# Kernel tuning notes

Hardware: AMD Instinct MI355X
Metric: run time of the kernel (lower is better)

## Reference

```python
import jax, jax.numpy as jnp
import numpy as np

DIM, HEADS, DFF = 768, 12, 3072
DK = DIM // HEADS
EPS = 1e-5

def _layernorm(x, w, b):
    mu = jnp.mean(x, axis=-1, keepdims=True)
    var = jnp.mean(jnp.square(x - mu), axis=-1, keepdims=True)
    return (x - mu) * jax.lax.rsqrt(var + EPS) * w + b

def setup_inputs() -> dict:
    key = jax.random.key(0)
    ks = jax.random.split(key, 5)
    B, N = 8, 1024
    std = 0.02
    return {
        "x": jax.random.normal(ks[0], (B, N, DIM), jnp.float32),
        "ln1_w": jnp.ones((DIM,), jnp.float32),
        "ln1_b": jnp.zeros((DIM,), jnp.float32),
        "qkv_w": jax.random.normal(ks[1], (3 * DIM, DIM), jnp.float32) * std,
        "qkv_b": jnp.zeros((3 * DIM,), jnp.float32),
        "proj_w": jax.random.normal(ks[2], (DIM, DIM), jnp.float32) * std,
        "proj_b": jnp.zeros((DIM,), jnp.float32),
        "ln2_w": jnp.ones((DIM,), jnp.float32),
        "ln2_b": jnp.zeros((DIM,), jnp.float32),
        "fc1_w": jax.random.normal(ks[3], (DFF, DIM), jnp.float32) * std,
        "fc1_b": jnp.zeros((DFF,), jnp.float32),
        "fc2_w": jax.random.normal(ks[4], (DIM, DFF), jnp.float32) * std,
        "fc2_b": jnp.zeros((DIM,), jnp.float32),
    }

def reference(x, ln1_w, ln1_b, qkv_w, qkv_b, proj_w, proj_b,
              ln2_w, ln2_b, fc1_w, fc1_b, fc2_w, fc2_b):
    B, N, C = x.shape
    # --- attention branch (pre-norm) ---
    h = _layernorm(x, ln1_w, ln1_b)
    qkv = h @ qkv_w.T + qkv_b                      # [B,N,3C]
    qkv = qkv.reshape(B, N, 3, HEADS, DK)
    q = qkv[:, :, 0].transpose(0, 2, 1, 3)         # [B,H,N,dk]
    k = qkv[:, :, 1].transpose(0, 2, 1, 3)
    v = qkv[:, :, 2].transpose(0, 2, 1, 3)
    scale = DK ** -0.5
    attn = jnp.einsum('bhnd,bhmd->bhnm', q, k) * scale
    attn = jax.nn.softmax(attn, axis=-1)
    out = jnp.einsum('bhnm,bhmd->bhnd', attn, v)   # [B,H,N,dk]
    out = out.transpose(0, 2, 1, 3).reshape(B, N, C)
    out = out @ proj_w.T + proj_b
    x = x + out
    # --- MLP branch (pre-norm) ---
    h = _layernorm(x, ln2_w, ln2_b)
    h = jax.nn.gelu(h @ fc1_w.T + fc1_b, approximate=False)
    h = h @ fc2_w.T + fc2_b
    return x + h
```

## Files before the change

### kernel.cpp

```cpp
#include <hip/hip_runtime.h>
#include <hip/hip_bf16.h>
#include <hip/hip_fp8.h>
#include <math.h>

typedef __attribute__((ext_vector_type(8))) __bf16 bf16x8;
typedef __attribute__((ext_vector_type(4))) __bf16 bf16x4;
typedef __attribute__((ext_vector_type(4))) float f32x4;
typedef __attribute__((ext_vector_type(4))) int i32x4;
typedef __attribute__((ext_vector_type(8))) int i32x8;

#define DIM 768
#define DFF 3072
#define HEADS 12
#define DKH 64
#define SEQ 1024
#define BATCH 8
#define ROWS (SEQ * BATCH)

#define GLD16(gp, lp)                                                      \
  __builtin_amdgcn_global_load_lds(                                        \
      (const __attribute__((address_space(1))) void*)(gp),                 \
      (__attribute__((address_space(3))) void*)(lp), 16, 0, 0)

__device__ __forceinline__ unsigned int pack4_e4m3(float a, float b, float c, float d) {
  __hip_fp8_e4m3 q0(a), q1(b), q2(c), q3(d);
  return (unsigned int)q0.__x | ((unsigned int)q1.__x << 8) |
         ((unsigned int)q2.__x << 16) | ((unsigned int)q3.__x << 24);
}

__global__ __launch_bounds__(256) void cvt4_kernel(const float* __restrict__ s0, int n0,
                                                   const float* __restrict__ s1, int n1,
                                                   const float* __restrict__ s2, int n2,
                                                   const float* __restrict__ s3, int n3,
                                                   __bf16* __restrict__ d0,
                                                   __bf16* __restrict__ d1,
                                                   unsigned char* __restrict__ d2,
                                                   unsigned char* __restrict__ d3) {
  int i0 = blockIdx.x * 256 + threadIdx.x;
  int st = gridDim.x * 256;
  const float* bsrc[2] = {s0, s1};
  __bf16* bdst[2] = {d0, d1};
  int bns[2] = {n0, n1};
#pragma unroll
  for (int t = 0; t < 2; ++t) {
    const f32x4* in = reinterpret_cast<const f32x4*>(bsrc[t]);
    bf16x4* out = reinterpret_cast<bf16x4*>(bdst[t]);
    for (int i = i0; i < bns[t]; i += st) {
      f32x4 v = in[i];
      bf16x4 o;
#pragma unroll
      for (int j = 0; j < 4; ++j) o[j] = (__bf16)v[j];
      out[i] = o;
    }
  }
  const float* fsrc[2] = {s2, s3};
  unsigned char* fdst[2] = {d2, d3};
  int fns[2] = {n2, n3};
#pragma unroll
  for (int t = 0; t < 2; ++t) {
    const f32x4* in = reinterpret_cast<const f32x4*>(fsrc[t]);
    unsigned int* out = reinterpret_cast<unsigned int*>(fdst[t]);
    for (int i = i0; i < fns[t]; i += st) {
      f32x4 v = in[i];
      out[i] = pack4_e4m3(v[0] * 16.f, v[1] * 16.f, v[2] * 16.f, v[3] * 16.f);
    }
  }
}

__global__ __launch_bounds__(256) void ln_kernel(const float* __restrict__ x,
                                                 const float* __restrict__ w,
                                                 const float* __restrict__ b,
                                                 __bf16* __restrict__ out) {
  int wid = threadIdx.x >> 6, lane = threadIdx.x & 63;
  int row = blockIdx.x * 4 + wid;
  const f32x4* xp = reinterpret_cast<const f32x4*>(x + (size_t)row * DIM);
  f32x4 v[3];
  float s1 = 0.f, s2 = 0.f;
#pragma unroll
  for (int i = 0; i < 3; ++i) {
    v[i] = xp[lane + i * 64];
#pragma unroll
    for (int c = 0; c < 4; ++c) { s1 += v[i][c]; s2 += v[i][c] * v[i][c]; }
  }
#pragma unroll
  for (int off = 1; off < 64; off <<= 1) {
    s1 += __shfl_xor(s1, off, 64);
    s2 += __shfl_xor(s2, off, 64);
  }
  float mu = s1 * (1.f / DIM);
  float var = s2 * (1.f / DIM) - mu * mu;
  float rs = rsqrtf(var + 1e-5f);
  const f32x4* wp = reinterpret_cast<const f32x4*>(w);
  const f32x4* bp = reinterpret_cast<const f32x4*>(b);
  __bf16* op = out + (size_t)row * DIM;
#pragma unroll
  for (int i = 0; i < 3; ++i) {
    int c4 = lane + i * 64;
    f32x4 wv = wp[c4], bv = bp[c4];
    bf16x4 ov;
#pragma unroll
    for (int c = 0; c < 4; ++c) ov[c] = (__bf16)((v[i][c] - mu) * rs * wv[c] + bv[c]);
    *reinterpret_cast<bf16x4*>(&op[c4 * 4]) = ov;
  }
}

__global__ __launch_bounds__(256) void ln_f8_kernel(const float* __restrict__ x,
                                                    const float* __restrict__ w,
                                                    const float* __restrict__ b,
                                                    unsigned char* __restrict__ out) {
  int wid = threadIdx.x >> 6, lane = threadIdx.x & 63;
  int row = blockIdx.x * 4 + wid;
  const f32x4* xp = reinterpret_cast<const f32x4*>(x + (size_t)row * DIM);
  f32x4 v[3];
  float s1 = 0.f, s2 = 0.f;
#pragma unroll
  for (int i = 0; i < 3; ++i) {
    v[i] = xp[lane + i * 64];
#pragma unroll
    for (int c = 0; c < 4; ++c) { s1 += v[i][c]; s2 += v[i][c] * v[i][c]; }
  }
#pragma unroll
  for (int off = 1; off < 64; off <<= 1) {
    s1 += __shfl_xor(s1, off, 64);
    s2 += __shfl_xor(s2, off, 64);
  }
  float mu = s1 * (1.f / DIM);
  float var = s2 * (1.f / DIM) - mu * mu;
  float rs = rsqrtf(var + 1e-5f);
  const f32x4* wp = reinterpret_cast<const f32x4*>(w);
  const f32x4* bp = reinterpret_cast<const f32x4*>(b);
  unsigned int* op = reinterpret_cast<unsigned int*>(out + (size_t)row * DIM);
#pragma unroll
  for (int i = 0; i < 3; ++i) {
    int c4 = lane + i * 64;
    f32x4 wv = wp[c4], bv = bp[c4];
    float o0 = (v[i][0] - mu) * rs * wv[0] + bv[0];
    float o1 = (v[i][1] - mu) * rs * wv[1] + bv[1];
    float o2 = (v[i][2] - mu) * rs * wv[2] + bv[2];
    float o3 = (v[i][3] - mu) * rs * wv[3] + bv[3];
    op[c4] = pack4_e4m3(o0, o1, o2, o3);
  }
}

template <int EPI, int BN, int DBUF>
__global__ __launch_bounds__(256) void gemm_nt(const __bf16* __restrict__ A,
                                               const __bf16* __restrict__ B,
                                               const float* __restrict__ bias,
                                               const float* __restrict__ resid,
                                               __bf16* __restrict__ vt,
                                               void* __restrict__ Cout,
                                               int M, int N, int K) {
  constexpr int NBUF = DBUF ? 2 : 1;
  constexpr int MF = (BN == 128) ? 4 : 2;
  __shared__ __bf16 As[NBUF * 128 * 64];
  __shared__ __bf16 Bs[NBUF * BN * 64];
  int tid = threadIdx.x;
  int bm = blockIdx.x, bn = blockIdx.y;
  int wid = tid >> 6, lane = tid & 63;
  int l15 = lane & 15, l4 = lane >> 4;
  int rowb = (BN == 128) ? (wid >> 1) * 64 : wid * 32;
  int colb = (BN == 128) ? (wid & 1) * 64 : 0;

  f32x4 acc[MF][4] = {};

  auto stage = [&](int buf, int kt) {
    __bf16* Ab = As + buf * 128 * 64;
    __bf16* Bb = Bs + buf * BN * 64;
#pragma unroll
    for (int r = 0; r < 4; ++r) {
      int c0 = (r * 4 + wid) * 64;
      int c = c0 + lane;
      int row = c >> 3;
      int colE = ((c & 7) ^ (row & 7)) * 8;
      GLD16(&A[(size_t)(bm * 128 + row) * K + kt + colE], &Ab[c0 * 8]);
    }
#pragma unroll
    for (int r = 0; r < BN / 32; ++r) {
      int c0 = (r * 4 + wid) * 64;
      int c = c0 + lane;
      int row = c >> 3;
      int colE = ((c & 7) ^ (row & 7)) * 8;
      GLD16(&B[(size_t)(bn * BN + row) * K + kt + colE], &Bb[c0 * 8]);
    }
  };

  auto compute = [&](int buf) {
    const __bf16* Ab = As + buf * 128 * 64;
    const __bf16* Bb = Bs + buf * BN * 64;
#pragma unroll
    for (int kc = 0; kc < 2; ++kc) {
      int cswz = ((kc * 4 + l4) ^ (l15 & 7)) * 8;
      bf16x8 af[MF], bfr[4];
#pragma unroll
      for (int m = 0; m < MF; ++m)
        af[m] = *reinterpret_cast<const bf16x8*>(&Ab[(rowb + m * 16 + l15) * 64 + cswz]);
#pragma unroll
      for (int n = 0; n < 4; ++n)
        bfr[n] = *reinterpret_cast<const bf16x8*>(&Bb[(colb + n * 16 + l15) * 64 + cswz]);
#pragma unroll
      for (int m = 0; m < MF; ++m)
#pragma unroll
        for (int n = 0; n < 4; ++n)
          acc[m][n] = __builtin_amdgcn_mfma_f32_16x16x32_bf16(af[m], bfr[n], acc[m][n], 0, 0, 0);
    }
  };

  if constexpr (DBUF) {
    stage(0, 0);
    __syncthreads();
    int cur = 0;
    for (int kt = 0; kt < K; kt += 64) {
      if (kt + 64 < K) stage(cur ^ 1, kt + 64);
      compute(cur);
      __syncthreads();
      cur ^= 1;
    }
  } else {
    for (int kt = 0; kt < K; kt += 64) {
      __syncthreads();
      stage(0, kt);
      __syncthreads();
      compute(0);
    }
  }

#pragma unroll
  for (int m = 0; m < MF; ++m)
#pragma unroll
    for (int n = 0; n < 4; ++n) {
      int row0 = bm * 128 + rowb + m * 16 + l4 * 4;
      int col = bn * BN + colb + n * 16 + l15;
      float bc = bias[col];
      if (EPI == 0 && col >= 2 * DIM) {
        int h = (col - 2 * DIM) >> 6, dk = (col - 2 * DIM) & 63;
        int b = row0 >> 10, tok = row0 & 1023;
        bf16x4 pk;
#pragma unroll
        for (int j = 0; j < 4; ++j) pk[j] = (__bf16)(acc[m][n][j] + bc);
        *reinterpret_cast<bf16x4*>(
            &vt[(size_t)((b * HEADS + h) * DKH + dk) * SEQ + tok]) = pk;
      } else {
#pragma unroll
        for (int j = 0; j < 4; ++j) {
          float v = acc[m][n][j] + bc;
          size_t idx = (size_t)(row0 + j) * N + col;
          if (EPI == 0) {
            ((__bf16*)Cout)[idx] = (__bf16)v;
          } else {
            ((float*)Cout)[idx] = v + resid[idx];
          }
        }
      }
    }
}

template <int EPI>
__global__ __launch_bounds__(256) void gemm_fp8(const unsigned char* __restrict__ A,
                                                const unsigned char* __restrict__ B,
                                                const float* __restrict__ bias,
                                                const float* __restrict__ resid,
                                                void* __restrict__ Cout,
                                                int M, int N, int K) {
  __shared__ unsigned char As[2 * 128 * 128];
  __shared__ unsigned char Bs[2 * 64 * 128];
  int tid = threadIdx.x;
  int bm = blockIdx.x, bn = blockIdx.y;
  int wid = tid >> 6, lane = tid & 63;
  int l15 = lane & 15, l4 = lane >> 4;
  int rowb = wid * 32;

  f32x4 acc[2][4] = {};

  auto stage = [&](int buf, int kt) {
    unsigned char* Ab = As + buf * 128 * 128;
    unsigned char* Bb = Bs + buf * 64 * 128;
#pragma unroll
    for (int r = 0; r < 4; ++r) {
      int c0 = (r * 4 + wid) * 64;
      int c = c0 + lane;
      int row = c >> 3;
      int j = (c & 7) ^ (row & 7);
      GLD16(&A[(size_t)(bm * 128 + row) * K + kt + j * 16], &Ab[c0 * 16]);
    }
#pragma unroll
    for (int r = 0; r < 2; ++r) {
      int c0 = (r * 4 + wid) * 64;
      int c = c0 + lane;
      int row = c >> 3;
      int j = (c & 7) ^ (row & 7);
      GLD16(&B[(size_t)(bn * 64 + row) * K + kt + j * 16], &Bb[c0 * 16]);
    }
  };

  auto ld32 = [&](const unsigned char* base, int row) -> i32x8 {
    int s7 = l15 & 7;
    i32x4 lo = *reinterpret_cast<const i32x4*>(&base[row * 128 + (((2 * l4) ^ s7) * 16)]);
    i32x4 hi = *reinterpret_cast<const i32x4*>(&base[row * 128 + (((2 * l4 + 1) ^ s7) * 16)]);
    i32x8 r;
    r[0] = lo[0]; r[1] = lo[1]; r[2] = lo[2]; r[3] = lo[3];
    r[4] = hi[0]; r[5] = hi[1]; r[6] = hi[2]; r[7] = hi[3];
    return r;
  };

  auto compute = [&](int buf) {
    const unsigned char* Ab = As + buf * 128 * 128;
    const unsigned char* Bb = Bs + buf * 64 * 128;
    i32x8 af[2], bfr[4];
#pragma unroll
    for (int m = 0; m < 2; ++m) af[m] = ld32(Ab, rowb + m * 16 + l15);
#pragma unroll
    for (int n = 0; n < 4; ++n) bfr[n] = ld32(Bb, n * 16 + l15);
#pragma unroll
    for (int m = 0; m < 2; ++m)
#pragma unroll
      for (int n = 0; n < 4; ++n)
        acc[m][n] = __builtin_amdgcn_mfma_scale_f32_16x16x128_f8f6f4(
            af[m], bfr[n], acc[m][n], 0, 0,
            0, 0x7F7F7F7F,
            0, 0x7F7F7F7F);
  };

  stage(0, 0);
  __syncthreads();
  int cur = 0;
  for (int kt = 0; kt < K; kt += 128) {
    if (kt + 128 < K) stage(cur ^ 1, kt + 128);
    compute(cur);
    __syncthreads();
    cur ^= 1;
  }

#pragma unroll
  for (int m = 0; m < 2; ++m)
#pragma unroll
    for (int n = 0; n < 4; ++n) {
      int row0 = bm * 128 + rowb + m * 16 + l4 * 4;
      int col = bn * 64 + n * 16 + l15;
      float bc = bias[col];
#pragma unroll
      for (int j = 0; j < 4; ++j) {
        if (EPI == 0) {
          float v = acc[m][n][j] * 0.0625f + bc;
          float z = 1.59576912f * (v + 0.044715f * v * v * v);
          float tt = __expf(fminf(z, 80.f));
          float g = v * __fdividef(tt, tt + 1.0f);
          ((unsigned char*)Cout)[(size_t)(row0 + j) * N + col] =
              __hip_fp8_e4m3(g * 16.f).__x;
        } else {
          size_t idx = (size_t)(row0 + j) * N + col;
          ((float*)Cout)[idx] = acc[m][n][j] * (1.f / 256.f) + bc + resid[idx];
        }
      }
    }
}

__global__ __launch_bounds__(256, 3) void attn_kernel(const __bf16* __restrict__ qkv,
                                                      const __bf16* __restrict__ vt,
                                                      __bf16* __restrict__ out) {
  int bid = blockIdx.x;
  int xcd = bid & 7, kk0 = bid >> 3;
  int bh = (kk0 >> 3) * 8 + xcd;
  int qt = kk0 & 7;
  int b = bh / HEADS, h = bh % HEADS;
  int tid = threadIdx.x, wid = tid >> 6, lane = tid & 63;
  int l15 = lane & 15, l4 = lane >> 4;
  int qr0 = qt * 128 + wid * 32;
  const size_t rs = 3 * DIM;
  const __bf16* Qb = qkv + (size_t)(b * SEQ) * rs + h * DKH;
  const __bf16* Kb = Qb + DIM;
  const __bf16* Vb = vt + (size_t)bh * DKH * SEQ;

  __shared__ __bf16 Ks[64 * 64];
  __shared__ __bf16 Vs[64 * 64];
  __shared__ __bf16 Ps[4][32][72];
  __bf16(*Psw)[72] = Ps[wid];

  bf16x8 qf[2][2];
#pragma unroll
  for (int m = 0; m < 2; ++m)
#pragma unroll
    for (int kc = 0; kc < 2; ++kc) {
      bf16x8 t = *reinterpret_cast<const bf16x8*>(
          &Qb[(size_t)(qr0 + m * 16 + l15) * rs + kc * 32 + l4 * 8]);
#pragma unroll
      for (int e = 0; e < 8; ++e) t[e] = (__bf16)((float)t[e] * 0.125f);
      qf[m][kc] = t;
    }

  f32x4 o[2][4] = {};
  f32x4 lsum[2] = {};

  for (int kv0 = 0; kv0 < SEQ; kv0 += 64) {
    __syncthreads();
#pragma unroll
    for (int cc = 0; cc < 2; ++cc) {
      int c0 = (wid * 2 + cc) * 64;
      int c = c0 + lane;
      int row = c >> 3;
      int sb = (c & 7) * 16;
      int pkc = sb ^ (((row >> 2) & 7) << 4);
      GLD16(&Kb[(size_t)(kv0 + row) * rs + (pkc >> 1)], &Ks[c0 * 8]);
      int pvc = sb ^ ((row & 7) << 4);
      GLD16(&Vb[(size_t)row * SEQ + kv0 + (pvc >> 1)], &Vs[c0 * 8]);
    }
    __syncthreads();

    bf16x8 kb[4][2];
#pragma unroll
    for (int nf = 0; nf < 4; ++nf)
#pragma unroll
      for (int kc = 0; kc < 2; ++kc) {
        int row = 4 * l15 + nf;
        int col = (kc * 64 + l4 * 16) ^ ((l15 & 7) << 4);
        kb[nf][kc] = *reinterpret_cast<const bf16x8*>(&Ks[row * 64 + (col >> 1)]);
      }
    f32x4 s[2][4] = {};
#pragma unroll
    for (int m = 0; m < 2; ++m)
#pragma unroll
      for (int nf = 0; nf < 4; ++nf)
#pragma unroll
        for (int kc = 0; kc < 2; ++kc)
          s[m][nf] = __builtin_amdgcn_mfma_f32_16x16x32_bf16(qf[m][kc], kb[nf][kc], s[m][nf], 0, 0, 0);

    bf16x8 vf[4][2];
#pragma unroll
    for (int d = 0; d < 4; ++d)
#pragma unroll
      for (int kc = 0; kc < 2; ++kc) {
        int row = d * 16 + l15;
        int col = (kc * 64 + l4 * 16) ^ ((l15 & 7) << 4);
        vf[d][kc] = *reinterpret_cast<const bf16x8*>(&Vs[row * 64 + (col >> 1)]);
      }

#pragma unroll
    for (int m = 0; m < 2; ++m)
#pragma unroll
      for (int j = 0; j < 4; ++j) {
        bf16x4 pk;
        float ss = 0.f;
#pragma unroll
        for (int nf = 0; nf < 4; ++nf) {
          float p = __expf(s[m][nf][j]);
          ss += p;
          pk[nf] = (__bf16)p;
        }
        lsum[m][j] += ss;
        *reinterpret_cast<bf16x4*>(&Psw[m * 16 + l4 * 4 + j][l15 * 4]) = pk;
      }
    asm volatile("s_waitcnt lgkmcnt(0)" ::: "memory");
    __builtin_amdgcn_sched_barrier(0);

    bf16x8 pf[2][2];
#pragma unroll
    for (int m = 0; m < 2; ++m)
#pragma unroll
      for (int kc = 0; kc < 2; ++kc)
        pf[m][kc] = *reinterpret_cast<const bf16x8*>(&Psw[m * 16 + l15][kc * 32 + l4 * 8]);
#pragma unroll
    for (int m = 0; m < 2; ++m)
#pragma unroll
      for (int d = 0; d < 4; ++d)
#pragma unroll
        for (int kc = 0; kc < 2; ++kc)
          o[m][d] = __builtin_amdgcn_mfma_f32_16x16x32_bf16(pf[m][kc], vf[d][kc], o[m][d], 0, 0, 0);
  }

#pragma unroll
  for (int off = 1; off < 16; off <<= 1)
#pragma unroll
    for (int m = 0; m < 2; ++m)
#pragma unroll
      for (int j = 0; j < 4; ++j) lsum[m][j] += __shfl_xor(lsum[m][j], off, 64);

  __bf16* op = out + (size_t)(b * SEQ) * DIM + h * DKH;
#pragma unroll
  for (int m = 0; m < 2; ++m)
#pragma unroll
    for (int j = 0; j < 4; ++j) {
      float rl = 1.f / lsum[m][j];
      int row = qr0 + m * 16 + l4 * 4 + j;
#pragma unroll
      for (int d = 0; d < 4; ++d)
        op[(size_t)row * DIM + d * 16 + l15] = (__bf16)(o[m][d][j] * rl);
    }
}

extern "C" void kernel_launch(void* const* d_in, const int* in_sizes, int n_in,
                              void* d_out, int out_size, void* d_ws, size_t ws_size,
                              hipStream_t stream) {
  const float* x      = (const float*)d_in[0];
  const float* ln1_w  = (const float*)d_in[1];
  const float* ln1_b  = (const float*)d_in[2];
  const float* qkv_w  = (const float*)d_in[3];
  const float* qkv_b  = (const float*)d_in[4];
  const float* proj_w = (const float*)d_in[5];
  const float* proj_b = (const float*)d_in[6];
  const float* ln2_w  = (const float*)d_in[7];
  const float* ln2_b  = (const float*)d_in[8];
  const float* fc1_w  = (const float*)d_in[9];
  const float* fc1_b  = (const float*)d_in[10];
  const float* fc2_w  = (const float*)d_in[11];
  const float* fc2_b  = (const float*)d_in[12];

  char* ws = (char*)d_ws;
  size_t o = 0;
  __bf16* qkvw_bf = (__bf16*)(ws + o); o += (size_t)3 * DIM * DIM * 2;
  __bf16* projw_bf = (__bf16*)(ws + o); o += (size_t)DIM * DIM * 2;
  unsigned char* fc1w_f8 = (unsigned char*)(ws + o); o += (size_t)DFF * DIM;
  unsigned char* fc2w_f8 = (unsigned char*)(ws + o); o += (size_t)DIM * DFF;
  __bf16* h_bf    = (__bf16*)(ws + o); o += (size_t)ROWS * DIM * 2;
  float*  x1      = (float*)(ws + o);  o += (size_t)ROWS * DIM * 4;
  __bf16* qkv_bf  = (__bf16*)(ws + o); o += (size_t)ROWS * 3 * DIM * 2;
  __bf16* attn_bf = (__bf16*)(ws + o); o += (size_t)ROWS * DIM * 2;
  unsigned char* ff_f8 = (unsigned char*)qkv_bf;
  __bf16* vtp     = (__bf16*)x1;
  unsigned char* h_f8 = (unsigned char*)h_bf;

  cvt4_kernel<<<2048, 256, 0, stream>>>(
      qkv_w, 3 * DIM * DIM / 4, proj_w, DIM * DIM / 4,
      fc1_w, DFF * DIM / 4, fc2_w, DIM * DFF / 4,
      qkvw_bf, projw_bf, fc1w_f8, fc2w_f8);

  ln_kernel<<<ROWS / 4, 256, 0, stream>>>(x, ln1_w, ln1_b, h_bf);
  gemm_nt<0, 64, 1><<<dim3(ROWS / 128, 3 * DIM / 64), 256, 0, stream>>>(
      h_bf, qkvw_bf, qkv_b, nullptr, vtp, qkv_bf, ROWS, 3 * DIM, DIM);
  attn_kernel<<<dim3(8 * BATCH * HEADS), 256, 0, stream>>>(qkv_bf, vtp, attn_bf);
  gemm_nt<2, 64, 1><<<dim3(ROWS / 128, DIM / 64), 256, 0, stream>>>(
      attn_bf, projw_bf, proj_b, x, nullptr, x1, ROWS, DIM, DIM);
  ln_f8_kernel<<<ROWS / 4, 256, 0, stream>>>(x1, ln2_w, ln2_b, h_f8);
  gemm_fp8<0><<<dim3(ROWS / 128, DFF / 64), 256, 0, stream>>>(
      h_f8, fc1w_f8, fc1_b, nullptr, ff_f8, ROWS, DFF, DIM);
  gemm_fp8<1><<<dim3(ROWS / 128, DIM / 64), 256, 0, stream>>>(
      ff_f8, fc2w_f8, fc2_b, x1, (float*)d_out, ROWS, DIM, DFF);
}
```

Measured before the change: 193.7 us.

## Triple-buffer GEMM k-loops with explicit vmcnt waits and XCD-aware block mapping

Replaces the double-buffered GEMM main loops (bf16 and fp8) with a three-stage LDS ring. Loads are issued two tiles ahead, and partial s_waitcnt vmcnt counts plus raw s_barrier calls replace full __syncthreads. It also flattens the 2D grid into 1D and remaps block IDs so that consecutive tiles land on the same XCD for L2 reuse, and raises wave priority during MFMA compute. The cost is more LDS per block (which may limit occupancy despite launch_bounds 2) and hand-tuned wait counts that must match the number of loads issued per stage.

Result: slower. 232.7 us (+20.1%).

```diff
diff --git a/kernel.cpp b/kernel.cpp
--- a/kernel.cpp
+++ b/kernel.cpp
@@ -26,6 +26,12 @@
   __hip_fp8_e4m3 q0(a), q1(b), q2(c), q3(d);
   return (unsigned int)q0.__x | ((unsigned int)q1.__x << 8) |
          ((unsigned int)q2.__x << 16) | ((unsigned int)q3.__x << 24);
+}
+
+__device__ __forceinline__ void xcd_map(int nbn, int& bm, int& bn) {
+  int wg = ((blockIdx.x & 7) * (gridDim.x >> 3)) + (blockIdx.x >> 3);
+  bm = wg / nbn;
+  bn = wg - bm * nbn;
 }
 
 __global__ __launch_bounds__(256) void cvt4_kernel(const float* __restrict__ s0, int n0,
@@ -142,30 +148,46 @@
   }
 }
 
-template <int EPI, int BN, int DBUF>
-__global__ __launch_bounds__(256) void gemm_nt(const __bf16* __restrict__ A,
-                                               const __bf16* __restrict__ B,
-                                               const float* __restrict__ bias,
-                                               const float* __restrict__ resid,
-                                               __bf16* __restrict__ vt,
-                                               void* __restrict__ Cout,
-                                               int M, int N, int K) {
-  constexpr int NBUF = DBUF ? 2 : 1;
-  constexpr int MF = (BN == 128) ? 4 : 2;
-  __shared__ __bf16 As[NBUF * 128 * 64];
-  __shared__ __bf16 Bs[NBUF * BN * 64];
+#define KSTEP(b0, b2, k, nk, BK)                                           \
+  do {                                                                     \
+    if ((k) + 2 < (nk)) {                                                  \
+      stage(b2, ((k) + 2) * (BK));                                         \
+      asm volatile("s_waitcnt vmcnt(12)" ::: "memory");                    \
+    } else if ((k) + 1 < (nk)) {                                           \
+      asm volatile("s_waitcnt vmcnt(6)" ::: "memory");                     \
+    } else {                                                               \
+      asm volatile("s_waitcnt vmcnt(0)" ::: "memory");                     \
+    }                                                                      \
+    __builtin_amdgcn_s_barrier();                                          \
+    __builtin_amdgcn_s_setprio(1);                                         \
+    compute(b0);                                                           \
+    __builtin_amdgcn_s_setprio(0);                                         \
+    asm volatile("s_waitcnt lgkmcnt(0)" ::: "memory");                     \
+    __builtin_amdgcn_s_barrier();                                          \
+  } while (0)
+
+template <int EPI>
+__global__ __launch_bounds__(256, 2) void gemm_nt(const __bf16* __restrict__ A,
+                                                  const __bf16* __restrict__ B,
+                                                  const float* __restrict__ bias,
+                                                  const float* __restrict__ resid,
+                                                  __bf16* __restrict__ vt,
+                                                  void* __restrict__ Cout,
+                                                  int M, int N, int K, int nbn) {
+  __shared__ __bf16 As[3 * 128 * 64];
+  __shared__ __bf16 Bs[3 * 64 * 64];
   int tid = threadIdx.x;
-  int bm = blockIdx.x, bn = blockIdx.y;
+  int bm, bn;
+  xcd_map(nbn, bm, bn);
   int wid = tid >> 6, lane = tid & 63;
   int l15 = lane & 15, l4 = lane >> 4;
-  int rowb = (BN == 128) ? (wid >> 1) * 64 : wid * 32;
-  int colb = (BN == 128) ? (wid & 1) * 64 : 0;
-
-  f32x4 acc[MF][4] = {};
+  int rowb = wid * 32;
+
+  f32x4 acc[2][4] = {};
 
   auto stage = [&](int buf, int kt) {
     __bf16* Ab = As + buf * 128 * 64;
-    __bf16* Bb = Bs + buf * BN * 64;
+    __bf16* Bb = Bs + buf * 64 * 64;
 #pragma unroll
     for (int r = 0; r < 4; ++r) {
       int c0 = (r * 4 + wid) * 64;
@@ -175,61 +197,51 @@
       GLD16(&A[(size_t)(bm * 128 + row) * K + kt + colE], &Ab[c0 * 8]);
     }
 #pragma unroll
-    for (int r = 0; r < BN / 32; ++r) {
+    for (int r = 0; r < 2; ++r) {
       int c0 = (r * 4 + wid) * 64;
       int c = c0 + lane;
       int row = c >> 3;
       int colE = ((c & 7) ^ (row & 7)) * 8;
-      GLD16(&B[(size_t)(bn * BN + row) * K + kt + colE], &Bb[c0 * 8]);
+      GLD16(&B[(size_t)(bn * 64 + row) * K + kt + colE], &Bb[c0 * 8]);
     }
   };
 
   auto compute = [&](int buf) {
     const __bf16* Ab = As + buf * 128 * 64;
-    const __bf16* Bb = Bs + buf * BN * 64;
+    const __bf16* Bb = Bs + buf * 64 * 64;
 #pragma unroll
     for (int kc = 0; kc < 2; ++kc) {
       int cswz = ((kc * 4 + l4) ^ (l15 & 7)) * 8;
-      bf16x8 af[MF], bfr[4];
-#pragma unroll
-      for (int m = 0; m < MF; ++m)
+      bf16x8 af[2], bfr[4];
+#pragma unroll
+      for (int m = 0; m < 2; ++m)
         af[m] = *reinterpret_cast<const bf16x8*>(&Ab[(rowb + m * 16 + l15) * 64 + cswz]);
 #pragma unroll
       for (int n = 0; n < 4; ++n)
-        bfr[n] = *reinterpret_cast<const bf16x8*>(&Bb[(colb + n * 16 + l15) * 64 + cswz]);
-#pragma unroll
-      for (int m = 0; m < MF; ++m)
+        bfr[n] = *reinterpret_cast<const bf16x8*>(&Bb[(n * 16 + l15) * 64 + cswz]);
+#pragma unroll
+      for (int m = 0; m < 2; ++m)
 #pragma unroll
         for (int n = 0; n < 4; ++n)
           acc[m][n] = __builtin_amdgcn_mfma_f32_16x16x32_bf16(af[m], bfr[n], acc[m][n], 0, 0, 0);
     }
   };
 
-  if constexpr (DBUF) {
-    stage(0, 0);
-    __syncthreads();
-    int cur = 0;
-    for (int kt = 0; kt < K; kt += 64) {
-      if (kt + 64 < K) stage(cur ^ 1, kt + 64);
-      compute(cur);
-      __syncthreads();
-      cur ^= 1;
-    }
-  } else {
-    for (int kt = 0; kt < K; kt += 64) {
-      __syncthreads();
-      stage(0, kt);
-      __syncthreads();
-      compute(0);
-    }
-  }
-
-#pragma unroll
-  for (int m = 0; m < MF; ++m)
+  int nk = K >> 6;
+  stage(0, 0);
+  stage(1, 64);
+  for (int k = 0; k < nk; k += 3) {
+    KSTEP(0, 2, k, nk, 64);
+    KSTEP(1, 0, k + 1, nk, 64);
+    KSTEP(2, 1, k + 2, nk, 64);
+  }
+
+#pragma unroll
+  for (int m = 0; m < 2; ++m)
 #pragma unroll
     for (int n = 0; n < 4; ++n) {
       int row0 = bm * 128 + rowb + m * 16 + l4 * 4;
-      int col = bn * BN + colb + n * 16 + l15;
+      int col = bn * 64 + n * 16 + l15;
       float bc = bias[col];
       if (EPI == 0 && col >= 2 * DIM) {
         int h = (col - 2 * DIM) >> 6, dk = (col - 2 * DIM) & 63;
@@ -255,16 +267,17 @@
 }
 
 template <int EPI>
-__global__ __launch_bounds__(256) void gemm_fp8(const unsigned char* __restrict__ A,
-                                                const unsigned char* __restrict__ B,
-                                                const float* __restrict__ bias,
-                                                const float* __restrict__ resid,
-                                                void* __restrict__ Cout,
-                                                int M, int N, int K) {
-  __shared__ unsigned char As[2 * 128 * 128];
-  __shared__ unsigned char Bs[2 * 64 * 128];
+__global__ __launch_bounds__(256, 2) void gemm_fp8(const unsigned char* __restrict__ A,
+                                                   const unsigned char* __restrict__ B,
+                                                   const float* __restrict__ bias,
+                                                   const float* __restrict__ resid,
+                                                   void* __restrict__ Cout,
+                                                   int M, int N, int K, int nbn) {
+  __shared__ unsigned char As[3 * 128 * 128];
+  __shared__ unsigned char Bs[3 * 64 * 128];
   int tid = threadIdx.x;
-  int bm = blockIdx.x, bn = blockIdx.y;
+  int bm, bn;
+  xcd_map(nbn, bm, bn);
   int wid = tid >> 6, lane = tid & 63;
   int l15 = lane & 15, l4 = lane >> 4;
   int rowb = wid * 32;
@@ -320,14 +333,13 @@
             0, 0x7F7F7F7F);
   };
 
+  int nk = K >> 7;
   stage(0, 0);
-  __syncthreads();
-  int cur = 0;
-  for (int kt = 0; kt < K; kt += 128) {
-    if (kt + 128 < K) stage(cur ^ 1, kt + 128);
-    compute(cur);
-    __syncthreads();
-    cur ^= 1;
+  stage(1, 128);
+  for (int k = 0; k < nk; k += 3) {
+    KSTEP(0, 2, k, nk, 128);
+    KSTEP(1, 0, k + 1, nk, 128);
+    KSTEP(2, 1, k + 2, nk, 128);
   }
 
 #pragma unroll
@@ -523,14 +535,14 @@
       qkvw_bf, projw_bf, fc1w_f8, fc2w_f8);
 
   ln_kernel<<<ROWS / 4, 256, 0, stream>>>(x, ln1_w, ln1_b, h_bf);
-  gemm_nt<0, 64, 1><<<dim3(ROWS / 128, 3 * DIM / 64), 256, 0, stream>>>(
-      h_bf, qkvw_bf, qkv_b, nullptr, vtp, qkv_bf, ROWS, 3 * DIM, DIM);
+  gemm_nt<0><<<dim3(2304), 256, 0, stream>>>(
+      h_bf, qkvw_bf, qkv_b, nullptr, vtp, qkv_bf, ROWS, 3 * DIM, DIM, 36);
   attn_kernel<<<dim3(8 * BATCH * HEADS), 256, 0, stream>>>(qkv_bf, vtp, attn_bf);
-  gemm_nt<2, 64, 1><<<dim3(ROWS / 128, DIM / 64), 256, 0, stream>>>(
-      attn_bf, projw_bf, proj_b, x, nullptr, x1, ROWS, DIM, DIM);
+  gemm_nt<2><<<dim3(768), 256, 0, stream>>>(
+      attn_bf, projw_bf, proj_b, x, nullptr, x1, ROWS, DIM, DIM, 12);
   ln_f8_kernel<<<ROWS / 4, 256, 0, stream>>>(x1, ln2_w, ln2_b, h_f8);
-  gemm_fp8<0><<<dim3(ROWS / 128, DFF / 64), 256, 0, stream>>>(
-      h_f8, fc1w_f8, fc1_b, nullptr, ff_f8, ROWS, DFF, DIM);
-  gemm_fp8<1><<<dim3(ROWS / 128, DIM / 64), 256, 0, stream>>>(
-      ff_f8, fc2w_f8, fc2_b, x1, (float*)d_out, ROWS, DIM, DFF);
-}
+  gemm_fp8<0><<<dim3(3072), 256, 0, stream>>>(
+      h_f8, fc1w_f8, fc1_b, nullptr, ff_f8, ROWS, DFF, DIM, 48);
+  gemm_fp8<1><<<dim3(768), 256, 0, stream>>>(
+      ff_f8, fc2w_f8, fc2_b, x1, (float*)d_out, ROWS, DIM, DFF, 12);
+}
```
